# Kernel optimization log

Hardware: AMD Instinct MI355X
Metric: run time of the kernel (lower is better)

The kernel has to match this reference:

```python
import jax, jax.numpy as jnp
import numpy as np

BN_EPS = 1e-5


def _gin_layer(x, src, dst, ew, eps, Wa, ba, Wb, bb, gamma, beta):
    # scatter-add aggregation: sum_j w_ij * x_j into node i
    msg = x[src] * ew[:, None]                       # [E, F]
    agg = jax.ops.segment_sum(msg, dst, num_segments=x.shape[0])  # [N, F]
    h = (1.0 + eps) * x + agg
    # MLP: Linear -> ReLU -> Linear -> BN(batch stats) -> ReLU
    h = jax.nn.relu(h @ Wa + ba)
    h = h @ Wb + bb
    mean = jnp.mean(h, axis=0)
    var = jnp.var(h, axis=0)
    h = (h - mean) * jax.lax.rsqrt(var + BN_EPS) * gamma + beta
    return jax.nn.relu(h)


def setup_inputs() -> dict:
    key = jax.random.key(0)
    N, E, F, H, L = 100000, 1600000, 128, 64, 3
    ks = jax.random.split(key, 12)
    x = jax.random.normal(ks[0], (N, F), dtype=jnp.float32)
    edge_index = jax.random.randint(ks[1], (2, E), 0, N, dtype=jnp.int64)
    edge_weight = jax.random.uniform(ks[2], (E,), dtype=jnp.float32)
    s = 0.05
    return {
        "x": x,
        "edge_index": edge_index,
        "edge_weight": edge_weight,
        # layer 1 (in_features -> hidden)
        "eps1": jnp.zeros((), jnp.float32),
        "W1a": jax.random.normal(ks[3], (F, H), jnp.float32) * s,
        "b1a": jnp.zeros((H,), jnp.float32),
        "W1b": jax.random.normal(ks[4], (H, H), jnp.float32) * s,
        "b1b": jnp.zeros((H,), jnp.float32),
        "g1": jnp.ones((H,), jnp.float32),
        "be1": jnp.zeros((H,), jnp.float32),
        # layers 2..L (hidden -> hidden), stacked on leading axis
        "epss": jnp.zeros((L - 1,), jnp.float32),
        "Wsa": jax.random.normal(ks[5], (L - 1, H, H), jnp.float32) * s,
        "bsa": jnp.zeros((L - 1, H), jnp.float32),
        "Wsb": jax.random.normal(ks[6], (L - 1, H, H), jnp.float32) * s,
        "bsb": jnp.zeros((L - 1, H), jnp.float32),
        "gs": jnp.ones((L - 1, H), jnp.float32),
        "bes": jnp.zeros((L - 1, H), jnp.float32),
    }


def reference(x, edge_index, edge_weight, eps1, W1a, b1a, W1b, b1b, g1, be1,
              epss, Wsa, bsa, Wsb, bsb, gs, bes):
    src, dst = edge_index[0], edge_index[1]
    h = _gin_layer(x, src, dst, edge_weight, eps1, W1a, b1a, W1b, b1b, g1, be1)
    for i in range(Wsa.shape[0]):
        h_new = _gin_layer(h, src, dst, edge_weight, epss[i],
                           Wsa[i], bsa[i], Wsb[i], bsb[i], gs[i], bes[i])
        h = h + h_new  # residual merge
    return h
```

## Files before the change

kernel.cpp:

```cpp
#include <hip/hip_runtime.h>

#define BN_EPS 1e-5f

typedef __attribute__((ext_vector_type(8))) short bf16x8;
typedef __attribute__((ext_vector_type(4))) float f32x4;

__device__ __forceinline__ unsigned short f32_to_bf16(float f) {
    unsigned u = __float_as_uint(f);
    u += 0x7fffu + ((u >> 16) & 1u);
    return (unsigned short)(u >> 16);
}
__device__ __forceinline__ float bf16_lo(unsigned v) { return __uint_as_float(v << 16); }
__device__ __forceinline__ float bf16_hi(unsigned v) { return __uint_as_float(v & 0xffff0000u); }

#define EW_SCALE (1.0f / 32767.0f)

__global__ __launch_bounds__(256) void rank_kernel(
    const int* __restrict__ dst, int* __restrict__ deg,
    int* __restrict__ rank, int E)
{
    int i = blockIdx.x * 256 + threadIdx.x;
    if (i < E) rank[i] = atomicAdd(&deg[dst[i]], 1);
}

__global__ __launch_bounds__(256) void scan_part1(
    const int* __restrict__ deg, int* __restrict__ blockSums, int N)
{
    __shared__ int sm[256];
    int t = threadIdx.x;
    int i0 = blockIdx.x * 512 + t * 2;
    int a = (i0     < N) ? deg[i0]     : 0;
    int b = (i0 + 1 < N) ? deg[i0 + 1] : 0;
    sm[t] = a + b;
    __syncthreads();
    for (int off = 128; off > 0; off >>= 1) {
        if (t < off) sm[t] += sm[t + off];
        __syncthreads();
    }
    if (t == 0) blockSums[blockIdx.x] = sm[0];
}

__global__ __launch_bounds__(256) void scan_part2(
    const int* __restrict__ blockSums, int* __restrict__ blockOff, int NB)
{
    __shared__ int sm[256];
    int t = threadIdx.x;
    sm[t] = (t < NB) ? blockSums[t] : 0;
    __syncthreads();
    for (int off = 1; off < 256; off <<= 1) {
        int v = (t >= off) ? sm[t - off] : 0;
        __syncthreads();
        sm[t] += v;
        __syncthreads();
    }
    if (t < NB) blockOff[t] = (t > 0) ? sm[t - 1] : 0;
}

__global__ __launch_bounds__(256) void scan_part3(
    const int* __restrict__ deg, const int* __restrict__ blockOff,
    int* __restrict__ row_start, int N, int E)
{
    __shared__ int sm[256];
    int t = threadIdx.x;
    int i0 = blockIdx.x * 512 + t * 2;
    int a = (i0     < N) ? deg[i0]     : 0;
    int b = (i0 + 1 < N) ? deg[i0 + 1] : 0;
    sm[t] = a + b;
    __syncthreads();
    for (int off = 1; off < 256; off <<= 1) {
        int v = (t >= off) ? sm[t - off] : 0;
        __syncthreads();
        sm[t] += v;
        __syncthreads();
    }
    int excl = blockOff[blockIdx.x] + ((t > 0) ? sm[t - 1] : 0);
    if (i0 < N)     row_start[i0]     = excl;
    if (i0 + 1 < N) row_start[i0 + 1] = excl + a;
    if (blockIdx.x == 0 && t == 0) row_start[N] = E;
}

__global__ __launch_bounds__(256) void fill_pass2(
    const int* __restrict__ src, const int* __restrict__ dst,
    const float* __restrict__ ew, const int* __restrict__ rank,
    const int* __restrict__ row_start, unsigned* __restrict__ einfo, int E)
{
    int i = blockIdx.x * 256 + threadIdx.x;
    if (i < E) {
        int pos = row_start[dst[i]] + rank[i];
        unsigned q = (unsigned)__float2int_rn(ew[i] * 32767.0f);
        einfo[pos] = ((unsigned)src[i] << 15) | q;
    }
}

__global__ __launch_bounds__(256) void prep_wfrag(
    const float* __restrict__ W1a, const float* __restrict__ W1b,
    const float* __restrict__ Wsa, const float* __restrict__ Wsb,
    unsigned short* __restrict__ wf, int* __restrict__ deg, int N, int nW)
{
    int z = blockIdx.x * 256 + threadIdx.x;
    if (z < N) deg[z] = 0;

    int bid = blockIdx.x;
    if (bid >= nW) return;
    const float* src; unsigned short* dst; int KS, chunk;
    if (bid < 4)      { src = W1a; dst = wf;        KS = 4; chunk = bid; }
    else if (bid < 6) { src = W1b; dst = wf + 8192; KS = 2; chunk = bid - 4; }
    else {
        int t = bid - 6;
        int layer = t >> 2;
        int wh = (t >> 1) & 1;
        chunk = t & 1;
        src = (wh ? Wsb : Wsa) + (size_t)layer * 4096;
        dst = wf + 12288 + layer * 8192 + wh * 4096;
        KS = 2;
    }
    int base = chunk * 2048;
    for (int e = base + threadIdx.x; e < base + 2048; e += 256) {
        int j  = e & 7;
        int l  = (e >> 3) & 63;
        int nk = e >> 9;
        int ks = nk % KS, n = nk / KS;
        int k  = ks * 32 + ((l >> 4) << 3) + j;
        int c  = n * 16 + (l & 15);
        dst[e] = f32_to_bf16(src[k * 64 + c]);
    }
}

template<int KS, int MODE, bool BF16OUT, bool STATS>
__global__ __launch_bounds__(256) void gemm_mfma(
    const void* __restrict__ Ain, const unsigned short* __restrict__ wfrag,
    const float* __restrict__ bias, void* __restrict__ out,
    float* __restrict__ statsOut,
    const float* __restrict__ statsIn, const float* __restrict__ g,
    const float* __restrict__ be, const float* __restrict__ res,
    float* __restrict__ hout, int N)
{
    constexpr int K   = KS * 32;
    constexpr int LDA = K + 8;
    __shared__ __align__(16) unsigned short sA[64 * LDA];
    __shared__ __align__(16) unsigned short sB[4 * KS * 64 * 8];
    __shared__ float sab[128];

    const int tid = threadIdx.x;

    if (MODE == 2) {
        if (tid < 64) {
            float invN = 1.0f / (float)N;
            float mean = statsIn[tid] * invN;
            float var  = statsIn[64 + tid] * invN - mean * mean;
            float a = g[tid] * rsqrtf(var + BN_EPS);
            sab[tid]      = a;
            sab[64 + tid] = be[tid] - mean * a;
        }
    }
    {
        const uint4* sv = (const uint4*)wfrag;
        uint4* dv = (uint4*)sB;
        for (int i = tid; i < 4 * KS * 64; i += 256) dv[i] = sv[i];
    }
    __syncthreads();

    const int w  = tid >> 6;
    const int l  = tid & 63;
    const int lr = l & 15;
    const int lg = l >> 4;
    const int ntiles = (N + 63) >> 6;

    for (int tile = blockIdx.x; tile < ntiles; tile += gridDim.x) {
        const int r0 = tile * 64;

        if (MODE == 1) {
            const uint4* Au = (const uint4*)Ain;
            constexpr int C16 = K / 8;
            for (int i = tid; i < 64 * C16; i += 256) {
                int r = i / C16, c = i % C16;
                uint4 v = make_uint4(0u, 0u, 0u, 0u);
                if (r0 + r < N) v = Au[(size_t)(r0 + r) * C16 + c];
                *reinterpret_cast<uint4*>(&sA[r * LDA + c * 8]) = v;
            }
        } else {
            const float* Af = (const float*)Ain;
            constexpr int C4 = K / 4;
            for (int i = tid; i < 64 * C4; i += 256) {
                int r = i / C4, c4 = i % C4;
                int gr = r0 + r;
                float4 v = make_float4(0.f, 0.f, 0.f, 0.f);
                if (gr < N) {
                    v = reinterpret_cast<const float4*>(Af + (size_t)gr * K)[c4];
                    if (MODE == 2) {
                        int l0 = c4 * 4;
                        v.x = fmaxf(fmaf(v.x, sab[l0 + 0], sab[64 + l0 + 0]), 0.f);
                        v.y = fmaxf(fmaf(v.y, sab[l0 + 1], sab[64 + l0 + 1]), 0.f);
                        v.z = fmaxf(fmaf(v.z, sab[l0 + 2], sab[64 + l0 + 2]), 0.f);
                        v.w = fmaxf(fmaf(v.w, sab[l0 + 3], sab[64 + l0 + 3]), 0.f);
                        if (res) {
                            float4 rv = reinterpret_cast<const float4*>(res + (size_t)gr * K)[c4];
                            v.x += rv.x; v.y += rv.y; v.z += rv.z; v.w += rv.w;
                        }
                        reinterpret_cast<float4*>(hout + (size_t)gr * K)[c4] = v;
                    }
                }
                ushort4 pk;
                pk.x = f32_to_bf16(v.x); pk.y = f32_to_bf16(v.y);
                pk.z = f32_to_bf16(v.z); pk.w = f32_to_bf16(v.w);
                *reinterpret_cast<ushort4*>(&sA[r * LDA + c4 * 4]) = pk;
            }
        }
        __syncthreads();

        f32x4 acc0 = {0.f,0.f,0.f,0.f}, acc1 = {0.f,0.f,0.f,0.f};
        f32x4 acc2 = {0.f,0.f,0.f,0.f}, acc3 = {0.f,0.f,0.f,0.f};

        #pragma unroll
        for (int ks = 0; ks < KS; ++ks) {
            bf16x8 af = *reinterpret_cast<const bf16x8*>(
                &sA[(w * 16 + lr) * LDA + ks * 32 + lg * 8]);
            bf16x8 b0 = *reinterpret_cast<const bf16x8*>(&sB[((0 * KS + ks) * 64 + l) * 8]);
            bf16x8 b1 = *reinterpret_cast<const bf16x8*>(&sB[((1 * KS + ks) * 64 + l) * 8]);
            bf16x8 b2 = *reinterpret_cast<const bf16x8*>(&sB[((2 * KS + ks) * 64 + l) * 8]);
            bf16x8 b3 = *reinterpret_cast<const bf16x8*>(&sB[((3 * KS + ks) * 64 + l) * 8]);
            acc0 = __builtin_amdgcn_mfma_f32_16x16x32_bf16(af, b0, acc0, 0, 0, 0);
            acc1 = __builtin_amdgcn_mfma_f32_16x16x32_bf16(af, b1, acc1, 0, 0, 0);
            acc2 = __builtin_amdgcn_mfma_f32_16x16x32_bf16(af, b2, acc2, 0, 0, 0);
            acc3 = __builtin_amdgcn_mfma_f32_16x16x32_bf16(af, b3, acc3, 0, 0, 0);
        }

        const int rlocal = w * 16 + lg * 4;
        float v[4][4], cs[4], cq[4];
        #pragma unroll
        for (int n = 0; n < 4; ++n) {
            float bv = bias ? bias[n * 16 + lr] : 0.f;
            f32x4 a = (n == 0) ? acc0 : (n == 1) ? acc1 : (n == 2) ? acc2 : acc3;
            cs[n] = 0.f; cq[n] = 0.f;
            #pragma unroll
            for (int j = 0; j < 4; ++j) {
                float vv = a[j] + bv;
                v[n][j] = vv;
                if (STATS && (r0 + rlocal + j < N)) { cs[n] += vv; cq[n] += vv * vv; }
            }
        }

        __syncthreads();

        if (BF16OUT) {
            #pragma unroll
            for (int n = 0; n < 4; ++n)
                #pragma unroll
                for (int j = 0; j < 4; ++j)
                    sA[(rlocal + j) * 72 + n * 16 + lr] = f32_to_bf16(v[n][j]);
            __syncthreads();
            unsigned short* o = (unsigned short*)out;
            for (int i = tid; i < 64 * 8; i += 256) {
                int r = i >> 3, q = i & 7;
                if (r0 + r < N)
                    *reinterpret_cast<uint4*>(o + (size_t)(r0 + r) * 64 + q * 8) =
                        *reinterpret_cast<const uint4*>(&sA[r * 72 + q * 8]);
            }
        } else {
            float* o = (float*)out;
            float* sAf = reinterpret_cast<float*>(sA);
            #pragma unroll
            for (int half = 0; half < 2; ++half) {
                if ((w >> 1) == half) {
                    #pragma unroll
                    for (int n = 0; n < 4; ++n)
                        #pragma unroll
                        for (int j = 0; j < 4; ++j)
                            sAf[((w & 1) * 16 + lg * 4 + j) * 68 + n * 16 + lr] = v[n][j];
                }
                __syncthreads();
                for (int i = tid; i < 32 * 16; i += 256) {
                    int r = i >> 4, c4 = i & 15;
                    int gr = r0 + half * 32 + r;
                    if (gr < N)
                        *reinterpret_cast<float4*>(o + (size_t)gr * 64 + c4 * 4) =
                            *reinterpret_cast<const float4*>(&sAf[r * 68 + c4 * 4]);
                }
                __syncthreads();
            }
        }

        if (STATS) {
            __syncthreads();
            float* red = reinterpret_cast<float*>(sA);
            int gg = w * 4 + lg;
            #pragma unroll
            for (int n = 0; n < 4; ++n) red[gg * 64 + n * 16 + lr] = cs[n];
            __syncthreads();
            if (tid < 64) {
                float s = 0.f;
                #pragma unroll
                for (int g2 = 0; g2 < 16; ++g2) s += red[g2 * 64 + tid];
                atomicAdd(&statsOut[tid], s);
            }
            __syncthreads();
            #pragma unroll
            for (int n = 0; n < 4; ++n) red[gg * 64 + n * 16 + lr] = cq[n];
            __syncthreads();
            if (tid < 64) {
                float q = 0.f;
                #pragma unroll
                for (int g2 = 0; g2 < 16; ++g2) q += red[g2 * 64 + tid];
                atomicAdd(&statsOut[64 + tid], q);
            }
        }
        __syncthreads();
    }
}

__global__ __launch_bounds__(256) void aggmid_kernel(
    const unsigned* __restrict__ yu,
    const int* __restrict__ row_start,
    const unsigned* __restrict__ einfo,
    const float* __restrict__ epsp,
    const float* __restrict__ ba,
    unsigned* __restrict__ midu, int N)
{
    const int lane = threadIdx.x & 63;
    const int half = lane >> 5;
    const int u    = lane & 31;
    int w  = (blockIdx.x * 256 + threadIdx.x) >> 6;
    const int nw = (gridDim.x * 256) >> 6;
    const float eps1 = 1.0f + epsp[0];
    const float2 bal = *reinterpret_cast<const float2*>(ba + 2 * u);

    for (int r = w; r < N; r += nw) {
        const int rs = row_start[r];
        const int re = row_start[r + 1];

        float a0 = 0.f, a1 = 0.f, b0 = 0.f, b1 = 0.f;
        float c0 = 0.f, c1 = 0.f, d0 = 0.f, d1 = 0.f;
        int j = rs;
        for (; j + 8 <= re; j += 8) {
            const int base = j + half * 4;
            unsigned p0 = einfo[base + 0];
            unsigned p1 = einfo[base + 1];
            unsigned p2 = einfo[base + 2];
            unsigned p3 = einfo[base + 3];
            unsigned y0 = yu[(size_t)(p0 >> 15) * 32 + u];
            unsigned y1 = yu[(size_t)(p1 >> 15) * 32 + u];
            unsigned y2 = yu[(size_t)(p2 >> 15) * 32 + u];
            unsigned y3 = yu[(size_t)(p3 >> 15) * 32 + u];
            float w0 = (float)(p0 & 0x7FFFu) * EW_SCALE;
            float w1 = (float)(p1 & 0x7FFFu) * EW_SCALE;
            float w2 = (float)(p2 & 0x7FFFu) * EW_SCALE;
            float w3 = (float)(p3 & 0x7FFFu) * EW_SCALE;
            a0 = fmaf(w0, bf16_lo(y0), a0); a1 = fmaf(w0, bf16_hi(y0), a1);
            b0 = fmaf(w1, bf16_lo(y1), b0); b1 = fmaf(w1, bf16_hi(y1), b1);
            c0 = fmaf(w2, bf16_lo(y2), c0); c1 = fmaf(w2, bf16_hi(y2), c1);
            d0 = fmaf(w3, bf16_lo(y3), d0); d1 = fmaf(w3, bf16_hi(y3), d1);
        }
        for (; j + 4 <= re; j += 4) {
            unsigned pA = einfo[j + half * 2 + 0];
            unsigned pB = einfo[j + half * 2 + 1];
            unsigned yA = yu[(size_t)(pA >> 15) * 32 + u];
            unsigned yB = yu[(size_t)(pB >> 15) * 32 + u];
            float wA = (float)(pA & 0x7FFFu) * EW_SCALE;
            float wB = (float)(pB & 0x7FFFu) * EW_SCALE;
            a0 = fmaf(wA, bf16_lo(yA), a0); a1 = fmaf(wA, bf16_hi(yA), a1);
            b0 = fmaf(wB, bf16_lo(yB), b0); b1 = fmaf(wB, bf16_hi(yB), b1);
        }
        for (; j < re; j += 2) {
            int e = j + half;
            bool valid = e < re;
            unsigned p = valid ? einfo[e] : 0u;
            float wv = valid ? (float)(p & 0x7FFFu) * EW_SCALE : 0.f;
            unsigned yv = yu[(size_t)(p >> 15) * 32 + u];
            a0 = fmaf(wv, bf16_lo(yv), a0); a1 = fmaf(wv, bf16_hi(yv), a1);
        }
        a0 = (a0 + b0) + (c0 + d0);
        a1 = (a1 + b1) + (c1 + d1);
        a0 += __shfl_xor(a0, 32);
        a1 += __shfl_xor(a1, 32);

        unsigned sv = yu[(size_t)r * 32 + u];
        float m0 = fmaf(eps1, bf16_lo(sv), a0) + bal.x;
        float m1 = fmaf(eps1, bf16_hi(sv), a1) + bal.y;
        if (half == 0) {
            unsigned pk = (unsigned)f32_to_bf16(fmaxf(m0, 0.f))
                        | ((unsigned)f32_to_bf16(fmaxf(m1, 0.f)) << 16);
            midu[(size_t)r * 32 + u] = pk;
        }
    }
}

template<int RES>
__global__ __launch_bounds__(256) void bn_apply(
    const float* __restrict__ h2, const float* __restrict__ stats,
    const float* __restrict__ g, const float* __restrict__ be,
    const float* res, float* out, int N, int n4)
{
    __shared__ float sab[128];
    int t = threadIdx.x;
    if (t < 64) {
        float invN = 1.0f / (float)N;
        float mean = stats[t] * invN;
        float var  = stats[64 + t] * invN - mean * mean;
        float a = g[t] * rsqrtf(var + BN_EPS);
        sab[t]      = a;
        sab[64 + t] = be[t] - mean * a;
    }
    __syncthreads();

    int i = blockIdx.x * blockDim.x + t;
    int stride = gridDim.x * blockDim.x;
    for (; i < n4; i += stride) {
        float4 v = reinterpret_cast<const float4*>(h2)[i];
        int l0 = (i * 4) & 63;
        float4 o;
        o.x = fmaxf(fmaf(v.x, sab[l0 + 0], sab[64 + l0 + 0]), 0.f);
        o.y = fmaxf(fmaf(v.y, sab[l0 + 1], sab[64 + l0 + 1]), 0.f);
        o.z = fmaxf(fmaf(v.z, sab[l0 + 2], sab[64 + l0 + 2]), 0.f);
        o.w = fmaxf(fmaf(v.w, sab[l0 + 3], sab[64 + l0 + 3]), 0.f);
        if (RES) {
            float4 rv = reinterpret_cast<const float4*>(res)[i];
            o.x += rv.x; o.y += rv.y; o.z += rv.z; o.w += rv.w;
        }
        reinterpret_cast<float4*>(out)[i] = o;
    }
}

extern "C" void kernel_launch(void* const* d_in, const int* in_sizes, int n_in,
                              void* d_out, int out_size, void* d_ws, size_t ws_size,
                              hipStream_t stream)
{
    const float* x    = (const float*)d_in[0];
    const int*   ei   = (const int*)  d_in[1];
    const float* ew   = (const float*)d_in[2];
    const float* eps1 = (const float*)d_in[3];
    const float* W1a  = (const float*)d_in[4];
    const float* b1a  = (const float*)d_in[5];
    const float* W1b  = (const float*)d_in[6];
    const float* b1b  = (const float*)d_in[7];
    const float* g1   = (const float*)d_in[8];
    const float* be1  = (const float*)d_in[9];
    const float* epss = (const float*)d_in[10];
    const float* Wsa  = (const float*)d_in[11];
    const float* bsa  = (const float*)d_in[12];
    const float* Wsb  = (const float*)d_in[13];
    const float* bsb  = (const float*)d_in[14];
    const float* gs   = (const float*)d_in[15];
    const float* bes  = (const float*)d_in[16];

    const int N   = in_sizes[0] / 128;
    const int E   = in_sizes[2];
    const int Lm1 = in_sizes[10];
    const int* src  = ei;
    const int* dstp = ei + E;

    char* ws = (char*)d_ws;
    size_t off = 0;
    unsigned* einfo = (unsigned*)(ws + off); off += (size_t)E * 4;
    float* regA  = (float*)(ws + off);   off += (size_t)N * 128 * 4;
    unsigned* ybf = (unsigned*)(ws + off); off += (size_t)N * 32 * 4;
    int*   rank  = (int*)  (ws + off);   off += (size_t)E * 4;
    int*   deg   = (int*)  (ws + off);   off += (size_t)N * 4;
    int*   row_start = (int*)(ws + off); off += (size_t)(N + 1) * 4;
    float* stats3 = (float*)(ws + off);  off += 384 * 4;
    int*   blockSums = (int*)(ws + off); off += 256 * 4;
    int*   blockOff  = (int*)(ws + off); off += 256 * 4;
    off = (off + 15) & ~(size_t)15;
    unsigned short* wf = (unsigned short*)(ws + off);
    float* outp  = (float*)d_out;
    float* bufY  = regA;
    unsigned* midu = (unsigned*)(regA + (size_t)N * 64);

    const int n4   = N * 64 / 4;
    const int NB   = (N + 511) / 512;
    const int EB   = (E + 255) / 256;
    const int nW   = 6 + 4 * Lm1;
    const int PREP_B = (N + 255) / 256;
    const int GB   = 512;

    prep_wfrag<<<PREP_B, 256, 0, stream>>>(W1a, W1b, Wsa, Wsb, wf, deg, N, nW);
    hipMemsetAsync(stats3, 0, 384 * 4, stream);

    rank_kernel<<<EB, 256, 0, stream>>>(dstp, deg, rank, E);
    scan_part1<<<NB, 256, 0, stream>>>(deg, blockSums, N);
    scan_part2<<<1, 256, 0, stream>>>(blockSums, blockOff, NB);
    scan_part3<<<NB, 256, 0, stream>>>(deg, blockOff, row_start, N, E);
    fill_pass2<<<EB, 256, 0, stream>>>(src, dstp, ew, rank, row_start, einfo, E);

    gemm_mfma<4, 0, true, false><<<GB, 256, 0, stream>>>(
        x, wf, nullptr, ybf, nullptr, nullptr, nullptr, nullptr, nullptr, nullptr, N);
    aggmid_kernel<<<2048, 256, 0, stream>>>(ybf, row_start, einfo, eps1, b1a, midu, N);
    gemm_mfma<2, 1, false, true><<<GB, 256, 0, stream>>>(
        midu, wf + 8192, b1b, bufY, stats3, nullptr, nullptr, nullptr, nullptr, nullptr, N);

    const float* pg  = g1;
    const float* pbe = be1;
    const float* resp = nullptr;
    for (int i = 0; i < Lm1; ++i) {
        const unsigned short* wfAi = wf + 12288 + i * 8192;
        const unsigned short* wfBi = wf + 12288 + i * 8192 + 4096;
        gemm_mfma<2, 2, true, false><<<GB, 256, 0, stream>>>(
            bufY, wfAi, nullptr, ybf, nullptr, stats3 + i * 128, pg, pbe, resp, outp, N);
        aggmid_kernel<<<2048, 256, 0, stream>>>(
            ybf, row_start, einfo, epss + i, bsa + (size_t)i * 64, midu, N);
        gemm_mfma<2, 1, false, true><<<GB, 256, 0, stream>>>(
            midu, wfBi, bsb + (size_t)i * 64, bufY, stats3 + (i + 1) * 128,
            nullptr, nullptr, nullptr, nullptr, nullptr, N);
        pg  = gs  + (size_t)i * 64;
        pbe = bes + (size_t)i * 64;
        resp = outp;
    }

    if (Lm1 > 0)
        bn_apply<1><<<2048, 256, 0, stream>>>(bufY, stats3 + Lm1 * 128, pg, pbe, outp, outp, N, n4);
    else
        bn_apply<0><<<2048, 256, 0, stream>>>(bufY, stats3, pg, pbe, nullptr, outp, N, n4);
}
```

Before: 483.1 us.

## Fuse rank counting into first GEMM and widen aggregation gather per lane

The edge rank/degree atomic counting now runs as extra blocks inside the first GEMM launch, so the two independent jobs share one grid. The stats memset is folded into the prep kernel. The aggregation kernel now has each lane load 8 bytes (4 bf16 features) and process 4 edges in parallel across 4 lane groups, reducing with two shuffles. This aims to remove launch overhead and raise memory-level parallelism in the gather, at the cost of more registers and a more complex tail path.

Measured after the change: 472.7 us. -2.1%, faster.

```diff
diff --git a/kernel.cpp b/kernel.cpp
--- a/kernel.cpp
+++ b/kernel.cpp
@@ -14,14 +14,6 @@
 __device__ __forceinline__ float bf16_hi(unsigned v) { return __uint_as_float(v & 0xffff0000u); }
 
 #define EW_SCALE (1.0f / 32767.0f)
-
-__global__ __launch_bounds__(256) void rank_kernel(
-    const int* __restrict__ dst, int* __restrict__ deg,
-    int* __restrict__ rank, int E)
-{
-    int i = blockIdx.x * 256 + threadIdx.x;
-    if (i < E) rank[i] = atomicAdd(&deg[dst[i]], 1);
-}
 
 __global__ __launch_bounds__(256) void scan_part1(
     const int* __restrict__ deg, int* __restrict__ blockSums, int N)
@@ -95,10 +87,12 @@
 __global__ __launch_bounds__(256) void prep_wfrag(
     const float* __restrict__ W1a, const float* __restrict__ W1b,
     const float* __restrict__ Wsa, const float* __restrict__ Wsb,
-    unsigned short* __restrict__ wf, int* __restrict__ deg, int N, int nW)
+    unsigned short* __restrict__ wf, int* __restrict__ deg,
+    float* __restrict__ stats3, int N, int nW)
 {
     int z = blockIdx.x * 256 + threadIdx.x;
     if (z < N) deg[z] = 0;
+    if (z < 384) stats3[z] = 0.f;
 
     int bid = blockIdx.x;
     if (bid >= nW) return;
@@ -133,7 +127,9 @@
     float* __restrict__ statsOut,
     const float* __restrict__ statsIn, const float* __restrict__ g,
     const float* __restrict__ be, const float* __restrict__ res,
-    float* __restrict__ hout, int N)
+    float* __restrict__ hout, int N,
+    const int* __restrict__ rdst, int* __restrict__ rdeg,
+    int* __restrict__ rrank, int rE, int gblocks)
 {
     constexpr int K   = KS * 32;
     constexpr int LDA = K + 8;
@@ -142,6 +138,13 @@
     __shared__ float sab[128];
 
     const int tid = threadIdx.x;
+    const int rankB = gridDim.x - gblocks;
+    if ((int)blockIdx.x < rankB) {
+        int i = blockIdx.x * 256 + tid;
+        if (i < rE) rrank[i] = atomicAdd(&rdeg[rdst[i]], 1);
+        return;
+    }
+    const int bid = blockIdx.x - rankB;
 
     if (MODE == 2) {
         if (tid < 64) {
@@ -166,7 +169,7 @@
     const int lg = l >> 4;
     const int ntiles = (N + 63) >> 6;
 
-    for (int tile = blockIdx.x; tile < ntiles; tile += gridDim.x) {
+    for (int tile = bid; tile < ntiles; tile += gblocks) {
         const int r0 = tile * 64;
 
         if (MODE == 1) {
@@ -317,69 +320,78 @@
     unsigned* __restrict__ midu, int N)
 {
     const int lane = threadIdx.x & 63;
-    const int half = lane >> 5;
-    const int u    = lane & 31;
+    const int q    = lane >> 4;
+    const int u    = lane & 15;
     int w  = (blockIdx.x * 256 + threadIdx.x) >> 6;
     const int nw = (gridDim.x * 256) >> 6;
     const float eps1 = 1.0f + epsp[0];
-    const float2 bal = *reinterpret_cast<const float2*>(ba + 2 * u);
+    const float4 bal = *reinterpret_cast<const float4*>(ba + 4 * u);
 
     for (int r = w; r < N; r += nw) {
         const int rs = row_start[r];
         const int re = row_start[r + 1];
 
-        float a0 = 0.f, a1 = 0.f, b0 = 0.f, b1 = 0.f;
-        float c0 = 0.f, c1 = 0.f, d0 = 0.f, d1 = 0.f;
+        float A0=0.f,A1=0.f,A2=0.f,A3=0.f, B0=0.f,B1=0.f,B2=0.f,B3=0.f;
+        float C0=0.f,C1=0.f,C2=0.f,C3=0.f, D0=0.f,D1=0.f,D2=0.f,D3=0.f;
         int j = rs;
-        for (; j + 8 <= re; j += 8) {
-            const int base = j + half * 4;
-            unsigned p0 = einfo[base + 0];
-            unsigned p1 = einfo[base + 1];
-            unsigned p2 = einfo[base + 2];
-            unsigned p3 = einfo[base + 3];
-            unsigned y0 = yu[(size_t)(p0 >> 15) * 32 + u];
-            unsigned y1 = yu[(size_t)(p1 >> 15) * 32 + u];
-            unsigned y2 = yu[(size_t)(p2 >> 15) * 32 + u];
-            unsigned y3 = yu[(size_t)(p3 >> 15) * 32 + u];
+        for (; j + 16 <= re; j += 16) {
+            const int b = j + q * 4;
+            unsigned p0 = einfo[b + 0], p1 = einfo[b + 1];
+            unsigned p2 = einfo[b + 2], p3 = einfo[b + 3];
+            uint2 y0 = *reinterpret_cast<const uint2*>(&yu[(size_t)(p0 >> 15) * 32 + 2 * u]);
+            uint2 y1 = *reinterpret_cast<const uint2*>(&yu[(size_t)(p1 >> 15) * 32 + 2 * u]);
+            uint2 y2 = *reinterpret_cast<const uint2*>(&yu[(size_t)(p2 >> 15) * 32 + 2 * u]);
+            uint2 y3 = *reinterpret_cast<const uint2*>(&yu[(size_t)(p3 >> 15) * 32 + 2 * u]);
             float w0 = (float)(p0 & 0x7FFFu) * EW_SCALE;
             float w1 = (float)(p1 & 0x7FFFu) * EW_SCALE;
             float w2 = (float)(p2 & 0x7FFFu) * EW_SCALE;
             float w3 = (float)(p3 & 0x7FFFu) * EW_SCALE;
-            a0 = fmaf(w0, bf16_lo(y0), a0); a1 = fmaf(w0, bf16_hi(y0), a1);
-            b0 = fmaf(w1, bf16_lo(y1), b0); b1 = fmaf(w1, bf16_hi(y1), b1);
-            c0 = fmaf(w2, bf16_lo(y2), c0); c1 = fmaf(w2, bf16_hi(y2), c1);
-            d0 = fmaf(w3, bf16_lo(y3), d0); d1 = fmaf(w3, bf16_hi(y3), d1);
+            A0 = fmaf(w0, bf16_lo(y0.x), A0); A1 = fmaf(w0, bf16_hi(y0.x), A1);
+            A2 = fmaf(w0, bf16_lo(y0.y), A2); A3 = fmaf(w0, bf16_hi(y0.y), A3);
+            B0 = fmaf(w1, bf16_lo(y1.x), B0); B1 = fmaf(w1, bf16_hi(y1.x), B1);
+            B2 = fmaf(w1, bf16_lo(y1.y), B2); B3 = fmaf(w1, bf16_hi(y1.y), B3);
+            C0 = fmaf(w2, bf16_lo(y2.x), C0); C1 = fmaf(w2, bf16_hi(y2.x), C1);
+            C2 = fmaf(w2, bf16_lo(y2.y), C2); C3 = fmaf(w2, bf16_hi(y2.y), C3);
+            D0 = fmaf(w3, bf16_lo(y3.x), D0); D1 = fmaf(w3, bf16_hi(y3.x), D1);
+            D2 = fmaf(w3, bf16_lo(y3.y), D2); D3 = fmaf(w3, bf16_hi(y3.y), D3);
         }
         for (; j + 4 <= re; j += 4) {
-            unsigned pA = einfo[j + half * 2 + 0];
-            unsigned pB = einfo[j + half * 2 + 1];
-            unsigned yA = yu[(size_t)(pA >> 15) * 32 + u];
-            unsigned yB = yu[(size_t)(pB >> 15) * 32 + u];
-            float wA = (float)(pA & 0x7FFFu) * EW_SCALE;
-            float wB = (float)(pB & 0x7FFFu) * EW_SCALE;
-            a0 = fmaf(wA, bf16_lo(yA), a0); a1 = fmaf(wA, bf16_hi(yA), a1);
-            b0 = fmaf(wB, bf16_lo(yB), b0); b1 = fmaf(wB, bf16_hi(yB), b1);
-        }
-        for (; j < re; j += 2) {
-            int e = j + half;
+            unsigned p = einfo[j + q];
+            uint2 y = *reinterpret_cast<const uint2*>(&yu[(size_t)(p >> 15) * 32 + 2 * u]);
+            float wv = (float)(p & 0x7FFFu) * EW_SCALE;
+            A0 = fmaf(wv, bf16_lo(y.x), A0); A1 = fmaf(wv, bf16_hi(y.x), A1);
+            A2 = fmaf(wv, bf16_lo(y.y), A2); A3 = fmaf(wv, bf16_hi(y.y), A3);
+        }
+        if (j < re) {
+            int e = j + q;
             bool valid = e < re;
-            unsigned p = valid ? einfo[e] : 0u;
+            unsigned p = einfo[valid ? e : rs];
             float wv = valid ? (float)(p & 0x7FFFu) * EW_SCALE : 0.f;
-            unsigned yv = yu[(size_t)(p >> 15) * 32 + u];
-            a0 = fmaf(wv, bf16_lo(yv), a0); a1 = fmaf(wv, bf16_hi(yv), a1);
-        }
-        a0 = (a0 + b0) + (c0 + d0);
-        a1 = (a1 + b1) + (c1 + d1);
-        a0 += __shfl_xor(a0, 32);
-        a1 += __shfl_xor(a1, 32);
-
-        unsigned sv = yu[(size_t)r * 32 + u];
-        float m0 = fmaf(eps1, bf16_lo(sv), a0) + bal.x;
-        float m1 = fmaf(eps1, bf16_hi(sv), a1) + bal.y;
-        if (half == 0) {
-            unsigned pk = (unsigned)f32_to_bf16(fmaxf(m0, 0.f))
-                        | ((unsigned)f32_to_bf16(fmaxf(m1, 0.f)) << 16);
-            midu[(size_t)r * 32 + u] = pk;
+            uint2 y = *reinterpret_cast<const uint2*>(&yu[(size_t)(p >> 15) * 32 + 2 * u]);
+            B0 = fmaf(wv, bf16_lo(y.x), B0); B1 = fmaf(wv, bf16_hi(y.x), B1);
+            B2 = fmaf(wv, bf16_lo(y.y), B2); B3 = fmaf(wv, bf16_hi(y.y), B3);
+        }
+        float s0 = (A0 + B0) + (C0 + D0);
+        float s1 = (A1 + B1) + (C1 + D1);
+        float s2 = (A2 + B2) + (C2 + D2);
+        float s3 = (A3 + B3) + (C3 + D3);
+        s0 += __shfl_xor(s0, 16); s0 += __shfl_xor(s0, 32);
+        s1 += __shfl_xor(s1, 16); s1 += __shfl_xor(s1, 32);
+        s2 += __shfl_xor(s2, 16); s2 += __shfl_xor(s2, 32);
+        s3 += __shfl_xor(s3, 16); s3 += __shfl_xor(s3, 32);
+
+        uint2 sv = *reinterpret_cast<const uint2*>(&yu[(size_t)r * 32 + 2 * u]);
+        float m0 = fmaf(eps1, bf16_lo(sv.x), s0) + bal.x;
+        float m1 = fmaf(eps1, bf16_hi(sv.x), s1) + bal.y;
+        float m2 = fmaf(eps1, bf16_lo(sv.y), s2) + bal.z;
+        float m3 = fmaf(eps1, bf16_hi(sv.y), s3) + bal.w;
+        if (q == 0) {
+            uint2 pk;
+            pk.x = (unsigned)f32_to_bf16(fmaxf(m0, 0.f))
+                 | ((unsigned)f32_to_bf16(fmaxf(m1, 0.f)) << 16);
+            pk.y = (unsigned)f32_to_bf16(fmaxf(m2, 0.f))
+                 | ((unsigned)f32_to_bf16(fmaxf(m3, 0.f)) << 16);
+            *reinterpret_cast<uint2*>(&midu[(size_t)r * 32 + 2 * u]) = pk;
         }
     }
 }
@@ -472,20 +484,21 @@
     const int PREP_B = (N + 255) / 256;
     const int GB   = 512;
 
-    prep_wfrag<<<PREP_B, 256, 0, stream>>>(W1a, W1b, Wsa, Wsb, wf, deg, N, nW);
-    hipMemsetAsync(stats3, 0, 384 * 4, stream);
-
-    rank_kernel<<<EB, 256, 0, stream>>>(dstp, deg, rank, E);
+    prep_wfrag<<<PREP_B, 256, 0, stream>>>(W1a, W1b, Wsa, Wsb, wf, deg, stats3, N, nW);
+
+    gemm_mfma<4, 0, true, false><<<EB + GB, 256, 0, stream>>>(
+        x, wf, nullptr, ybf, nullptr, nullptr, nullptr, nullptr, nullptr, nullptr, N,
+        dstp, deg, rank, E, GB);
+
     scan_part1<<<NB, 256, 0, stream>>>(deg, blockSums, N);
     scan_part2<<<1, 256, 0, stream>>>(blockSums, blockOff, NB);
     scan_part3<<<NB, 256, 0, stream>>>(deg, blockOff, row_start, N, E);
     fill_pass2<<<EB, 256, 0, stream>>>(src, dstp, ew, rank, row_start, einfo, E);
 
-    gemm_mfma<4, 0, true, false><<<GB, 256, 0, stream>>>(
-        x, wf, nullptr, ybf, nullptr, nullptr, nullptr, nullptr, nullptr, nullptr, N);
     aggmid_kernel<<<2048, 256, 0, stream>>>(ybf, row_start, einfo, eps1, b1a, midu, N);
     gemm_mfma<2, 1, false, true><<<GB, 256, 0, stream>>>(
-        midu, wf + 8192, b1b, bufY, stats3, nullptr, nullptr, nullptr, nullptr, nullptr, N);
+        midu, wf + 8192, b1b, bufY, stats3, nullptr, nullptr, nullptr, nullptr, nullptr, N,
+        nullptr, nullptr, nullptr, 0, GB);
 
     const float* pg  = g1;
     const float* pbe = be1;
@@ -494,12 +507,14 @@
         const unsigned short* wfAi = wf + 12288 + i * 8192;
         const unsigned short* wfBi = wf + 12288 + i * 8192 + 4096;
         gemm_mfma<2, 2, true, false><<<GB, 256, 0, stream>>>(
-            bufY, wfAi, nullptr, ybf, nullptr, stats3 + i * 128, pg, pbe, resp, outp, N);
+            bufY, wfAi, nullptr, ybf, nullptr, stats3 + i * 128, pg, pbe, resp, outp, N,
+            nullptr, nullptr, nullptr, 0, GB);
         aggmid_kernel<<<2048, 256, 0, stream>>>(
             ybf, row_start, einfo, epss + i, bsa + (size_t)i * 64, midu, N);
         gemm_mfma<2, 1, false, true><<<GB, 256, 0, stream>>>(
             midu, wfBi, bsb + (size_t)i * 64, bufY, stats3 + (i + 1) * 128,
-            nullptr, nullptr, nullptr, nullptr, nullptr, N);
+            nullptr, nullptr, nullptr, nullptr, nullptr, N,
+            nullptr, nullptr, nullptr, 0, GB);
         pg  = gs  + (size_t)i * 64;
         pbe = bes + (size_t)i * 64;
         resp = outp;
```
